# Performance work log

Hardware: AMD Instinct MI355X
Metric: run time of the kernel (lower is better)

The kernel has to match this reference:

```python
import jax, jax.numpy as jnp
import numpy as np

N_NODES = 50000
N_EDGES = 800000
D_IN = 256
D_OUT = 256
BN_EPS = 1e-5


def setup_inputs() -> dict:
    key = jax.random.key(0)
    k1, k2, k3 = jax.random.split(key, 3)
    x = jax.random.normal(k1, (N_NODES, D_IN), dtype=jnp.float32)
    edge_index = jax.random.randint(k2, (2, N_EDGES), 0, N_NODES, dtype=jnp.int64)
    # GCNConv linear weight [out, in] (glorot-ish scale), separate bias
    W = jax.random.normal(k3, (D_OUT, D_IN), dtype=jnp.float32) * (1.0 / np.sqrt(D_IN))
    bias = jnp.zeros((D_OUT,), dtype=jnp.float32)
    gamma = jnp.ones((D_OUT,), dtype=jnp.float32)
    beta = jnp.zeros((D_OUT,), dtype=jnp.float32)
    return {"x": x, "edge_index": edge_index, "W": W, "bias": bias, "gamma": gamma, "beta": beta}


def reference(x, edge_index, W, bias, gamma, beta):
    N = x.shape[0]
    self_loops = jnp.arange(N, dtype=edge_index.dtype)
    row = jnp.concatenate([edge_index[0], self_loops])  # source nodes
    col = jnp.concatenate([edge_index[1], self_loops])  # target nodes

    # linear transform first (PyG GCNConv order): [N, D_out]
    h = x @ W.T

    # symmetric degree normalization with self-loops
    deg = jax.ops.segment_sum(jnp.ones_like(col, dtype=h.dtype), col, num_segments=N)
    dinv = jnp.where(deg > 0, jax.lax.rsqrt(deg), 0.0)
    norm = dinv[row] * dinv[col]  # [E+N]

    # gather -> scale -> scatter-add
    msg = h[row] * norm[:, None]                         # [E+N, D_out]
    agg = jax.ops.segment_sum(msg, col, num_segments=N)  # [N, D_out]
    agg = agg + bias

    # BatchNorm (training mode: batch stats over nodes, biased var)
    mean = jnp.mean(agg, axis=0)
    var = jnp.mean((agg - mean) ** 2, axis=0)
    y = gamma * (agg - mean) * jax.lax.rsqrt(var + BN_EPS) + beta
    return jax.nn.relu(y)
```

## Files before the change

### kernel.cpp

```cpp
#include <hip/hip_runtime.h>
#include <cstdio>

#define NN 50000
#define NE 800000
#define DD 256
#define WS_NEED 113080000UL

__attribute__((constructor)) static void r24_on_load(void) {
    fprintf(stderr, "R24SO_LOADED\n");
    fflush(stderr);
}

__device__ float b2f(unsigned short u) {
    union { unsigned int i; float f; } c;
    c.i = ((unsigned int)u) << 16;
    return c.f;
}
__device__ float clampf(float v) { return fminf(fmaxf(v, -65504.f), 65504.f); }
__device__ float rdF(const void* p, long long idx, int ff) {
    if (ff) return clampf(b2f(((const unsigned short*)p)[idx]));
    return clampf(((const float*)p)[idx]);
}
__device__ unsigned short f2b_rne(float f) {
    union { float f; unsigned int u; } c;
    c.f = f;
    unsigned int r = (c.u + 0x7FFFu + ((c.u >> 16) & 1u)) >> 16;
    return (unsigned short)r;
}

typedef __attribute__((ext_vector_type(8))) short bf16x8;
typedef __attribute__((ext_vector_type(4))) float f32x4;
typedef __attribute__((ext_vector_type(4))) _Float16 f16x4;
typedef __attribute__((ext_vector_type(8))) _Float16 f16x8;

__device__ int detect_ff(const unsigned short* xr) {
    __shared__ int dacc;
    if (threadIdx.x == 0) dacc = 0;
    __syncthreads();
    int g = 0;
    for (int j = 0; j < 4; j++) {
        unsigned short u = xr[(threadIdx.x * 4 + j) * 2];
        int e = (u >> 7) & 0xFF;
        if (u == 0 || u == 0x8000 || (e >= 100 && e <= 140)) g++;
    }
    atomicAdd(&dacc, g);
    __syncthreads();
    return dacc >= 922;
}

__global__ void k_setup(int* deg, int* misc, const unsigned short* xr,
                        const int* ei, int* flags, const void* W, const void* bias,
                        const void* gamma, const void* beta, unsigned short* Wb,
                        float* pf) {
    int b = blockIdx.x;
    int t = threadIdx.x;
    if (b < 196) {
        int i = b * 256 + t;
        if (i < NN) deg[i] = 0;
        if (i < 16) misc[i] = 0;
        return;
    }
    if (b == 196) {
        __shared__ int acc2;
        if (t == 0) acc2 = 0;
        int ff = detect_ff(xr);
        if (ei[2 * t + 1] != 0) atomicAdd(&acc2, 1);
        __syncthreads();
        if (t == 0) {
            flags[0] = ff;
            flags[1] = (acc2 == 0) ? 1 : 0;
        }
        pf[t] = rdF(bias, t, ff);
        pf[DD + t] = rdF(gamma, t, ff);
        pf[2 * DD + t] = rdF(beta, t, ff);
        return;
    }
    int ff = detect_ff(xr);
    int i = (b - 197) * 256 + t;
    Wb[i] = f2b_rne(rdF(W, i, ff));
}

__global__ void k_edges(const int* raw, const int* flags, int* deg) {
    int e = blockIdx.x * 256 + threadIdx.x;
    if (e >= NE) return;
    int f = flags[1];
    int r = f ? raw[2 * e] : raw[e];
    int c = f ? raw[2 * (NE + e)] : raw[NE + e];
    if ((unsigned int)r < NN && (unsigned int)c < NN) atomicAdd(&deg[c], 1);
}

__global__ __launch_bounds__(256) void k_alloc(const int* deg, int* off, int* cursor,
                                               float* dinv, int* gcur) {
    __shared__ int sm[256];
    __shared__ int sbase;
    int tid = threadIdx.x;
    int i = blockIdx.x * 256 + tid;
    int v = (i < NN) ? deg[i] : 0;
    sm[tid] = v;
    __syncthreads();
    for (int s = 1; s < 256; s <<= 1) {
        int t = (tid >= s) ? sm[tid - s] : 0;
        __syncthreads();
        sm[tid] += t;
        __syncthreads();
    }
    if (tid == 255) sbase = atomicAdd(gcur, sm[255]);
    __syncthreads();
    if (i < NN) {
        int o = sbase + sm[tid] - v;
        off[i] = o;
        cursor[i] = o;
        dinv[i] = rsqrtf((float)(v + 1));
    }
}

#define WP 264
__global__ __launch_bounds__(1024) void k_gemm(const void* x, const int* flags,
                                               const unsigned short* Wb,
                                               const float* dinv, _Float16* h) {
    __shared__ unsigned short wlds[256 * WP];
    int t = threadIdx.x;

#pragma unroll
    for (int i = 0; i < 8; i++) {
        int c = t + i * 1024;
        int row = c >> 5;
        int off = (c & 31) * 8;
        bf16x8 v = *(const bf16x8*)(Wb + row * DD + off);
        *(bf16x8*)(&wlds[row * WP + off]) = v;
    }
    __syncthreads();

    int wave = t >> 6;
    int lane = t & 63;
    int rw = blockIdx.x * 16 + wave;
    if (rw >= 3125) return;
    int r0 = rw * 16;
    int l15 = lane & 15;
    int kq = lane >> 4;

    bf16x8 a[8];
    int ff = flags[0];
    if (ff) {
        const unsigned short* p =
            (const unsigned short*)x + (unsigned long long)(r0 + l15) * DD + kq * 8;
#pragma unroll
        for (int k = 0; k < 8; k++)
            a[k] = *(const bf16x8*)(p + k * 32);
    } else {
        const float* p = (const float*)x + (unsigned long long)(r0 + l15) * DD + kq * 8;
#pragma unroll
        for (int k = 0; k < 8; k++) {
#pragma unroll
            for (int j = 0; j < 8; j++)
                a[k][j] = (short)f2b_rne(p[k * 32 + j]);
        }
    }

    float dv[4];
#pragma unroll
    for (int j = 0; j < 4; j++) dv[j] = dinv[r0 + kq * 4 + j];

#pragma unroll
    for (int ct = 0; ct < 16; ct++) {
        f32x4 acc = {0.f, 0.f, 0.f, 0.f};
#pragma unroll
        for (int k = 0; k < 8; k++) {
            bf16x8 b = *(const bf16x8*)(&wlds[(ct * 16 + l15) * WP + kq * 8 + k * 32]);
            acc = __builtin_amdgcn_mfma_f32_16x16x32_bf16(a[k], b, acc, 0, 0, 0);
        }
        _Float16* op = h + (unsigned long long)(r0 + kq * 4) * DD + ct * 16 + l15;
#pragma unroll
        for (int j = 0; j < 4; j++)
            op[(unsigned long long)j * DD] = (_Float16)(acc[j] * dv[j]);
    }
}

__global__ void k_fill(const int* raw, const int* flags, int* cursor, int* csrc) {
    int e = blockIdx.x * 256 + threadIdx.x;
    if (e >= NE) return;
    int f = flags[1];
    int r = f ? raw[2 * e] : raw[e];
    int c = f ? raw[2 * (NE + e)] : raw[NE + e];
    if ((unsigned int)c < NN && (unsigned int)r < NN) {
        int slot = atomicAdd(&cursor[c], 1);
        if ((unsigned int)slot < NE) csrc[slot] = r;
    }
}

__global__ __launch_bounds__(256) void g_agg(const _Float16* h, const float* dinv,
                                             const int* off, const int* deg,
                                             const int* csrc, const float* pf,
                                             _Float16* agg) {
    int lane = threadIdx.x & 63;
    int n = blockIdx.x * 4 + (threadIdx.x >> 6);
    int f0 = lane * 4;
    int s = __builtin_amdgcn_readfirstlane(off[n]);
    int cnt = __builtin_amdgcn_readfirstlane(deg[n]);
    float dn = dinv[n];
    f16x4 hv = *(const f16x4*)(h + (unsigned long long)n * DD + f0);
    float a0 = (float)hv[0];
    float a1 = (float)hv[1];
    float a2 = (float)hv[2];
    float a3 = (float)hv[3];
    const int* ip = csrc + s;
    int k = 0;
    for (; k + 8 <= cnt; k += 8) {
        int i0 = ip[k + 0], i1 = ip[k + 1], i2 = ip[k + 2], i3 = ip[k + 3];
        int i4 = ip[k + 4], i5 = ip[k + 5], i6 = ip[k + 6], i7 = ip[k + 7];
        f16x4 v0 = *(const f16x4*)(h + (unsigned long long)i0 * DD + f0);
        f16x4 v1 = *(const f16x4*)(h + (unsigned long long)i1 * DD + f0);
        f16x4 v2 = *(const f16x4*)(h + (unsigned long long)i2 * DD + f0);
        f16x4 v3 = *(const f16x4*)(h + (unsigned long long)i3 * DD + f0);
        f16x4 v4 = *(const f16x4*)(h + (unsigned long long)i4 * DD + f0);
        f16x4 v5 = *(const f16x4*)(h + (unsigned long long)i5 * DD + f0);
        f16x4 v6 = *(const f16x4*)(h + (unsigned long long)i6 * DD + f0);
        f16x4 v7 = *(const f16x4*)(h + (unsigned long long)i7 * DD + f0);
        a0 += (((float)v0[0] + (float)v1[0]) + ((float)v2[0] + (float)v3[0])) +
              (((float)v4[0] + (float)v5[0]) + ((float)v6[0] + (float)v7[0]));
        a1 += (((float)v0[1] + (float)v1[1]) + ((float)v2[1] + (float)v3[1])) +
              (((float)v4[1] + (float)v5[1]) + ((float)v6[1] + (float)v7[1]));
        a2 += (((float)v0[2] + (float)v1[2]) + ((float)v2[2] + (float)v3[2])) +
              (((float)v4[2] + (float)v5[2]) + ((float)v6[2] + (float)v7[2]));
        a3 += (((float)v0[3] + (float)v1[3]) + ((float)v2[3] + (float)v3[3])) +
              (((float)v4[3] + (float)v5[3]) + ((float)v6[3] + (float)v7[3]));
    }
    for (; k + 4 <= cnt; k += 4) {
        int i0 = ip[k + 0], i1 = ip[k + 1], i2 = ip[k + 2], i3 = ip[k + 3];
        f16x4 v0 = *(const f16x4*)(h + (unsigned long long)i0 * DD + f0);
        f16x4 v1 = *(const f16x4*)(h + (unsigned long long)i1 * DD + f0);
        f16x4 v2 = *(const f16x4*)(h + (unsigned long long)i2 * DD + f0);
        f16x4 v3 = *(const f16x4*)(h + (unsigned long long)i3 * DD + f0);
        a0 += ((float)v0[0] + (float)v1[0]) + ((float)v2[0] + (float)v3[0]);
        a1 += ((float)v0[1] + (float)v1[1]) + ((float)v2[1] + (float)v3[1]);
        a2 += ((float)v0[2] + (float)v1[2]) + ((float)v2[2] + (float)v3[2]);
        a3 += ((float)v0[3] + (float)v1[3]) + ((float)v2[3] + (float)v3[3]);
    }
    for (; k < cnt; k++) {
        int i0 = ip[k];
        f16x4 v0 = *(const f16x4*)(h + (unsigned long long)i0 * DD + f0);
        a0 += (float)v0[0];
        a1 += (float)v0[1];
        a2 += (float)v0[2];
        a3 += (float)v0[3];
    }
    f16x4 o;
    o[0] = (_Float16)(dn * a0 + pf[f0 + 0]);
    o[1] = (_Float16)(dn * a1 + pf[f0 + 1]);
    o[2] = (_Float16)(dn * a2 + pf[f0 + 2]);
    o[3] = (_Float16)(dn * a3 + pf[f0 + 3]);
    *(f16x4*)(agg + (unsigned long long)n * DD + f0) = o;
}

__global__ __launch_bounds__(256) void k_stats1(const _Float16* agg, float* pstat) {
    __shared__ float ls[2][DD];
    int t = threadIdx.x;
    int rg = t >> 5;
    int cg = t & 31;
    float s[8], s2[8];
#pragma unroll
    for (int j = 0; j < 8; j++) { s[j] = 0.f; s2[j] = 0.f; }
    int row0 = blockIdx.x * 64;
    int rend = row0 + 64;
    if (rend > NN) rend = NN;
    for (int r = row0 + rg; r < rend; r += 8) {
        f16x8 v = *(const f16x8*)(agg + (unsigned long long)r * DD + cg * 8);
#pragma unroll
        for (int j = 0; j < 8; j++) {
            float f = (float)v[j];
            s[j] += f;
            s2[j] += f * f;
        }
    }
    ls[0][t] = 0.f;
    ls[1][t] = 0.f;
    __syncthreads();
#pragma unroll
    for (int j = 0; j < 8; j++) {
        atomicAdd(&ls[0][cg * 8 + j], s[j]);
        atomicAdd(&ls[1][cg * 8 + j], s2[j]);
    }
    __syncthreads();
    float* pb = pstat + (unsigned long long)blockIdx.x * 512;
    pb[t] = ls[0][t];
    pb[256 + t] = ls[1][t];
}

__global__ __launch_bounds__(256) void k_stats2(const float* pstat, const float* pf,
                                                float* ss) {
    __shared__ float ls[16][16];
    int t = threadIdx.x;
    int r = t >> 4;
    int c = t & 15;
    int j = blockIdx.x;
    int slot = (c < 8) ? (j * 8 + c) : (256 + j * 8 + (c - 8));
    float acc = 0.f;
    for (int b = r; b < 782; b += 16)
        acc += pstat[(unsigned long long)b * 512 + slot];
    ls[r][c] = acc;
    __syncthreads();
    for (int step = 8; step >= 1; step >>= 1) {
        if (r < step) ls[r][c] += ls[r + step][c];
        __syncthreads();
    }
    if (t < 8) {
        int f = j * 8 + t;
        float sv = ls[0][t];
        float sv2 = ls[0][t + 8];
        float mean = sv * (1.0f / NN);
        float var = fmaxf(sv2 * (1.0f / NN) - mean * mean, 0.f);
        float sc = pf[DD + f] * rsqrtf(var + 1e-5f);
        ss[f] = sc;
        ss[DD + f] = pf[2 * DD + f] - mean * sc;
    }
}

__global__ void DenseGCNLayer_2937757631000_kernel(const _Float16* agg, const float* ss,
                                                   float* out) {
    int t = threadIdx.x;
    unsigned long long base =
        (unsigned long long)blockIdx.x * 2048 + (unsigned int)t * 8;
    int f = (int)(base & 255);
    f16x8 v = *(const f16x8*)(agg + base);
    f32x4 o0, o1;
#pragma unroll
    for (int j = 0; j < 4; j++)
        o0[j] = fmaxf(ss[f + j] * (float)v[j] + ss[DD + f + j], 0.f);
#pragma unroll
    for (int j = 0; j < 4; j++)
        o1[j] = fmaxf(ss[f + 4 + j] * (float)v[4 + j] + ss[DD + f + 4 + j], 0.f);
    *(f32x4*)(out + base) = o0;
    *(f32x4*)(out + base + 4) = o1;
}

extern "C" void kernel_launch(void* const* d_in, const int* in_sizes, int n_in,
                              void* d_out, int out_size, void* d_ws, size_t ws_size,
                              hipStream_t stream) {
    const void* x = d_in[0];
    const int* ei = (const int*)d_in[1];
    const void* W = d_in[2];
    const void* bias = d_in[3];
    const void* gamma = d_in[4];
    const void* beta = d_in[5];
    char* ws = (char*)d_ws;
    float* out = (float*)d_out;

    _Float16* h = (_Float16*)(ws + 0UL);
    _Float16* agg = (_Float16*)(ws + 51200000UL);
    float* pstat = (float*)(ws + 102400000UL);
    int* csrc = (int*)(ws + 108800000UL);
    unsigned short* Wb = (unsigned short*)(ws + 112000000UL);
    int* deg = (int*)(ws + 112262144UL);
    float* dinv = (float*)(ws + 112462336UL);
    int* off = (int*)(ws + 112662528UL);
    int* cursor = (int*)(ws + 112862720UL);
    int* misc = (int*)(ws + 113063936UL);
    float* pf = (float*)(ws + 113064960UL);
    float* ss = (float*)(ws + 113070080UL);
    int* flags = (int*)(ws + 113072128UL);

    if (ws_size < WS_NEED) {
        fprintf(stderr, "R24_WS_SMALL %zu\n", ws_size);
        fflush(stderr);
        return;
    }

    k_setup<<<453, 256, 0, stream>>>(deg, misc, (const unsigned short*)x, ei,
                                     flags, W, bias, gamma, beta, Wb, pf);
    k_edges<<<3125, 256, 0, stream>>>(ei, flags, deg);
    k_alloc<<<196, 256, 0, stream>>>(deg, off, cursor, dinv, &misc[0]);
    k_gemm<<<196, 1024, 0, stream>>>(x, flags, Wb, dinv, h);
    k_fill<<<3125, 256, 0, stream>>>(ei, flags, cursor, csrc);
    g_agg<<<12500, 256, 0, stream>>>(h, dinv, off, deg, csrc, pf, agg);
    k_stats1<<<782, 256, 0, stream>>>(agg, pstat);
    k_stats2<<<32, 256, 0, stream>>>(pstat, pf, ss);
    DenseGCNLayer_2937757631000_kernel<<<6250, 256, 0, stream>>>(agg, ss, out);
}
```

Measured before the change: 322.2 us.

## Replace CSR build with fixed-capacity per-node buckets plus overflow list

Edges are now bucketed in a single pass into fixed 32-slot per-node arrays, with a global overflow list for any slots beyond that. This drops the separate degree-count pass over the edges and the prefix-scan allocation kernel; a small kernel computes dinv from the counts. The aggregation kernel reads neighbours from the fixed slot region and, for nodes that overflowed, scans the whole overflow list. The cost is a larger, padded index array and a linear overflow scan whenever a node has more than 32 in-edges, which is rare for these random graphs.

```diff
diff --git a/kernel.cpp b/kernel.cpp
--- a/kernel.cpp
+++ b/kernel.cpp
@@ -4,10 +4,11 @@
 #define NN 50000
 #define NE 800000
 #define DD 256
+#define CAP 32
 #define WS_NEED 113080000UL
 
-__attribute__((constructor)) static void r24_on_load(void) {
-    fprintf(stderr, "R24SO_LOADED\n");
+__attribute__((constructor)) static void r25_on_load(void) {
+    fprintf(stderr, "R25SO_LOADED\n");
     fflush(stderr);
 }
 
@@ -48,7 +49,7 @@
     return dacc >= 922;
 }
 
-__global__ void k_setup(int* deg, int* misc, const unsigned short* xr,
+__global__ void k_setup(int* cnt, int* misc, const unsigned short* xr,
                         const int* ei, int* flags, const void* W, const void* bias,
                         const void* gamma, const void* beta, unsigned short* Wb,
                         float* pf) {
@@ -56,7 +57,7 @@
     int t = threadIdx.x;
     if (b < 196) {
         int i = b * 256 + t;
-        if (i < NN) deg[i] = 0;
+        if (i < NN) cnt[i] = 0;
         if (i < 16) misc[i] = 0;
         return;
     }
@@ -80,38 +81,28 @@
     Wb[i] = f2b_rne(rdF(W, i, ff));
 }
 
-__global__ void k_edges(const int* raw, const int* flags, int* deg) {
+__global__ void k_fill1(const int* raw, const int* flags, int* cnt, int* csrc,
+                        int* ovf, int* novf) {
     int e = blockIdx.x * 256 + threadIdx.x;
     if (e >= NE) return;
     int f = flags[1];
     int r = f ? raw[2 * e] : raw[e];
     int c = f ? raw[2 * (NE + e)] : raw[NE + e];
-    if ((unsigned int)r < NN && (unsigned int)c < NN) atomicAdd(&deg[c], 1);
-}
-
-__global__ __launch_bounds__(256) void k_alloc(const int* deg, int* off, int* cursor,
-                                               float* dinv, int* gcur) {
-    __shared__ int sm[256];
-    __shared__ int sbase;
-    int tid = threadIdx.x;
-    int i = blockIdx.x * 256 + tid;
-    int v = (i < NN) ? deg[i] : 0;
-    sm[tid] = v;
-    __syncthreads();
-    for (int s = 1; s < 256; s <<= 1) {
-        int t = (tid >= s) ? sm[tid - s] : 0;
-        __syncthreads();
-        sm[tid] += t;
-        __syncthreads();
-    }
-    if (tid == 255) sbase = atomicAdd(gcur, sm[255]);
-    __syncthreads();
-    if (i < NN) {
-        int o = sbase + sm[tid] - v;
-        off[i] = o;
-        cursor[i] = o;
-        dinv[i] = rsqrtf((float)(v + 1));
-    }
+    if ((unsigned int)c < NN && (unsigned int)r < NN) {
+        int slot = atomicAdd(&cnt[c], 1);
+        if (slot < CAP) {
+            csrc[c * CAP + slot] = r;
+        } else {
+            int o = atomicAdd(novf, 1);
+            ovf[2 * o] = c;
+            ovf[2 * o + 1] = r;
+        }
+    }
+}
+
+__global__ void k_dinv(const int* cnt, float* dinv) {
+    int i = blockIdx.x * 256 + threadIdx.x;
+    if (i < NN) dinv[i] = rsqrtf((float)(cnt[i] + 1));
 }
 
 #define WP 264
@@ -176,36 +167,24 @@
     }
 }
 
-__global__ void k_fill(const int* raw, const int* flags, int* cursor, int* csrc) {
-    int e = blockIdx.x * 256 + threadIdx.x;
-    if (e >= NE) return;
-    int f = flags[1];
-    int r = f ? raw[2 * e] : raw[e];
-    int c = f ? raw[2 * (NE + e)] : raw[NE + e];
-    if ((unsigned int)c < NN && (unsigned int)r < NN) {
-        int slot = atomicAdd(&cursor[c], 1);
-        if ((unsigned int)slot < NE) csrc[slot] = r;
-    }
-}
-
 __global__ __launch_bounds__(256) void g_agg(const _Float16* h, const float* dinv,
-                                             const int* off, const int* deg,
-                                             const int* csrc, const float* pf,
-                                             _Float16* agg) {
+                                             const int* cnt, const int* csrc,
+                                             const int* ovf, const int* novf,
+                                             const float* pf, _Float16* agg) {
     int lane = threadIdx.x & 63;
     int n = blockIdx.x * 4 + (threadIdx.x >> 6);
     int f0 = lane * 4;
-    int s = __builtin_amdgcn_readfirstlane(off[n]);
-    int cnt = __builtin_amdgcn_readfirstlane(deg[n]);
+    int cn = __builtin_amdgcn_readfirstlane(cnt[n]);
+    int m = (cn < CAP) ? cn : CAP;
     float dn = dinv[n];
     f16x4 hv = *(const f16x4*)(h + (unsigned long long)n * DD + f0);
     float a0 = (float)hv[0];
     float a1 = (float)hv[1];
     float a2 = (float)hv[2];
     float a3 = (float)hv[3];
-    const int* ip = csrc + s;
+    const int* ip = csrc + n * CAP;
     int k = 0;
-    for (; k + 8 <= cnt; k += 8) {
+    for (; k + 8 <= m; k += 8) {
         int i0 = ip[k + 0], i1 = ip[k + 1], i2 = ip[k + 2], i3 = ip[k + 3];
         int i4 = ip[k + 4], i5 = ip[k + 5], i6 = ip[k + 6], i7 = ip[k + 7];
         f16x4 v0 = *(const f16x4*)(h + (unsigned long long)i0 * DD + f0);
@@ -225,7 +204,7 @@
         a3 += (((float)v0[3] + (float)v1[3]) + ((float)v2[3] + (float)v3[3])) +
               (((float)v4[3] + (float)v5[3]) + ((float)v6[3] + (float)v7[3]));
     }
-    for (; k + 4 <= cnt; k += 4) {
+    for (; k + 4 <= m; k += 4) {
         int i0 = ip[k + 0], i1 = ip[k + 1], i2 = ip[k + 2], i3 = ip[k + 3];
         f16x4 v0 = *(const f16x4*)(h + (unsigned long long)i0 * DD + f0);
         f16x4 v1 = *(const f16x4*)(h + (unsigned long long)i1 * DD + f0);
@@ -236,13 +215,26 @@
         a2 += ((float)v0[2] + (float)v1[2]) + ((float)v2[2] + (float)v3[2]);
         a3 += ((float)v0[3] + (float)v1[3]) + ((float)v2[3] + (float)v3[3]);
     }
-    for (; k < cnt; k++) {
+    for (; k < m; k++) {
         int i0 = ip[k];
         f16x4 v0 = *(const f16x4*)(h + (unsigned long long)i0 * DD + f0);
         a0 += (float)v0[0];
         a1 += (float)v0[1];
         a2 += (float)v0[2];
         a3 += (float)v0[3];
+    }
+    if (cn > CAP) {
+        int no = __builtin_amdgcn_readfirstlane(*novf);
+        for (int i = 0; i < no; i++) {
+            if (ovf[2 * i] == n) {
+                int r = ovf[2 * i + 1];
+                f16x4 v0 = *(const f16x4*)(h + (unsigned long long)r * DD + f0);
+                a0 += (float)v0[0];
+                a1 += (float)v0[1];
+                a2 += (float)v0[2];
+                a3 += (float)v0[3];
+            }
+        }
     }
     f16x4 o;
     o[0] = (_Float16)(dn * a0 + pf[f0 + 0]);
@@ -347,31 +339,29 @@
 
     _Float16* h = (_Float16*)(ws + 0UL);
     _Float16* agg = (_Float16*)(ws + 51200000UL);
+    int* ovf = (int*)(ws + 80000000UL);
     float* pstat = (float*)(ws + 102400000UL);
-    int* csrc = (int*)(ws + 108800000UL);
+    int* csrc = (int*)(ws + 104800000UL);
     unsigned short* Wb = (unsigned short*)(ws + 112000000UL);
-    int* deg = (int*)(ws + 112262144UL);
+    int* cnt = (int*)(ws + 112262144UL);
     float* dinv = (float*)(ws + 112462336UL);
-    int* off = (int*)(ws + 112662528UL);
-    int* cursor = (int*)(ws + 112862720UL);
     int* misc = (int*)(ws + 113063936UL);
     float* pf = (float*)(ws + 113064960UL);
     float* ss = (float*)(ws + 113070080UL);
     int* flags = (int*)(ws + 113072128UL);
 
     if (ws_size < WS_NEED) {
-        fprintf(stderr, "R24_WS_SMALL %zu\n", ws_size);
+        fprintf(stderr, "R25_WS_SMALL %zu\n", ws_size);
         fflush(stderr);
         return;
     }
 
-    k_setup<<<453, 256, 0, stream>>>(deg, misc, (const unsigned short*)x, ei,
+    k_setup<<<453, 256, 0, stream>>>(cnt, misc, (const unsigned short*)x, ei,
                                      flags, W, bias, gamma, beta, Wb, pf);
-    k_edges<<<3125, 256, 0, stream>>>(ei, flags, deg);
-    k_alloc<<<196, 256, 0, stream>>>(deg, off, cursor, dinv, &misc[0]);
+    k_fill1<<<3125, 256, 0, stream>>>(ei, flags, cnt, csrc, ovf, &misc[0]);
+    k_dinv<<<196, 256, 0, stream>>>(cnt, dinv);
     k_gemm<<<196, 1024, 0, stream>>>(x, flags, Wb, dinv, h);
-    k_fill<<<3125, 256, 0, stream>>>(ei, flags, cursor, csrc);
-    g_agg<<<12500, 256, 0, stream>>>(h, dinv, off, deg, csrc, pf, agg);
+    g_agg<<<12500, 256, 0, stream>>>(h, dinv, cnt, csrc, ovf, &misc[0], pf, agg);
     k_stats1<<<782, 256, 0, stream>>>(agg, pstat);
     k_stats2<<<32, 256, 0, stream>>>(pstat, pf, ss);
     DenseGCNLayer_2937757631000_kernel<<<6250, 256, 0, stream>>>(agg, ss, out);
```

After: 288.1 us. 10.6% less time.
